# Kernel optimization log

Hardware: AMD Instinct MI355X
Metric: run time of the kernel (lower is better)

## Reference

```python
import jax, jax.numpy as jnp
import numpy as np

EMBED_DIM = 584  # module-global, used as softmax scale base (C ** -0.5)


def setup_inputs() -> dict:
    key = jax.random.key(0)
    ks = jax.random.split(key, 7)
    B, T, C, H, D = 16, 1024, 584, 8, 73
    x = jax.random.normal(ks[0], (B, T, C), dtype=jnp.float32)
    memory = jax.random.normal(ks[1], (B, T, C), dtype=jnp.float32)
    s = 0.02
    Wq = jax.random.normal(ks[2], (H, C, D), dtype=jnp.float32) * s
    Wk = jax.random.normal(ks[3], (H, C, D), dtype=jnp.float32) * s
    Wv = jax.random.normal(ks[4], (H, C, D), dtype=jnp.float32) * s
    Wp = jax.random.normal(ks[5], (C, C), dtype=jnp.float32) * s
    bp = jnp.zeros((C,), dtype=jnp.float32)
    return {"x": x, "memory": memory, "Wq": Wq, "Wk": Wk, "Wv": Wv, "Wp": Wp, "bp": bp}


def reference(x, memory, Wq, Wk, Wv, Wp, bp):
    B, T, C = x.shape
    # per-head projections, vectorized over heads: [B, H, T, D]
    q = jnp.einsum('btc,hcd->bhtd', x, Wq)
    k = jnp.einsum('bsc,hcd->bhsd', memory, Wk)
    v = jnp.einsum('btc,hcd->bhtd', x, Wv)  # NOTE: value from x, per original code
    # scale uses full embed dim C (not head size), per original code
    scores = jnp.einsum('bhtd,bhsd->bhts', q, k) * (C ** -0.5)
    weights = jax.nn.softmax(scores, axis=-1)
    # dropout is identity in eval/reference mode
    out = jnp.einsum('bhts,bhsd->bhtd', weights, v)  # requires S == T (matches original)
    out = out.transpose(0, 2, 1, 3).reshape(B, T, C)  # concat heads on last dim
    out = out @ Wp + bp  # output projection (dropout identity)
    return out
```

## Files before the change

kernel.cpp:

```cpp
#include <hip/hip_runtime.h>
#include <hip/hip_bf16.h>

typedef unsigned short u16;
typedef __attribute__((ext_vector_type(4))) unsigned short u16x4;
typedef __attribute__((ext_vector_type(8))) unsigned short u16x8;
typedef __attribute__((ext_vector_type(8))) __bf16 bf16x8;
typedef __attribute__((ext_vector_type(4))) float f32x4;

#define BB 16
#define TSEQ 1024
#define CC 584
#define HH 8
#define DHD 73
#define NR (BB*TSEQ)
#define KPW 640
#define DP 96
#define HD (HH*DP)
#define NP3 768
#define PPITCH 88
#define CEXP 0.0596985934f

__device__ __forceinline__ u16 f2bf(float f) {
  __bf16 h = (__bf16)f;
  return __builtin_bit_cast(u16, h);
}
__device__ __forceinline__ bf16x8 as_bf(u16x8 v) { return __builtin_bit_cast(bf16x8, v); }

#define GLL16(g, l) __builtin_amdgcn_global_load_lds( \
    (const __attribute__((address_space(1))) void*)(g), \
    (__attribute__((address_space(3))) void*)(l), 16, 0, 0)

#define BARRIER() asm volatile("s_barrier" ::: "memory")
#define VMW7()    asm volatile("s_waitcnt vmcnt(7)" ::: "memory")
#define VMW2()    asm volatile("s_waitcnt vmcnt(2)" ::: "memory")
#define VMW0()    asm volatile("s_waitcnt vmcnt(0)" ::: "memory")

#define PKA 10240
#define PKB2 720
#define PKC2 240
__global__ void pack_all_kernel(const float* __restrict__ x, const float* __restrict__ mem,
                                const float* __restrict__ Wq, const float* __restrict__ Wk,
                                const float* __restrict__ Wv, const float* __restrict__ Wp,
                                u16* __restrict__ xmb, u16* __restrict__ wt,
                                u16* __restrict__ wpt) {
  const int bidx = blockIdx.x;
  const int tid = threadIdx.x;
  if (bidx < PKA) {
    int idx = bidx * 256 + tid;
    int row = idx / (KPW / 8);
    int c8  = (idx % (KPW / 8)) * 8;
    u16x8 o = {0, 0, 0, 0, 0, 0, 0, 0};
    if (c8 < CC) {
      const float* src = (row < NR) ? &x[(size_t)row * CC + c8]
                                    : &mem[(size_t)(row - NR) * CC + c8];
      f32x4 a = *(const f32x4*)src;
      f32x4 b = *(const f32x4*)(src + 4);
#pragma unroll
      for (int t = 0; t < 4; t++) { o[t] = f2bf(a[t]); o[4 + t] = f2bf(b[t]); }
    }
    *(u16x8*)&xmb[(size_t)row * KPW + c8] = o;
  } else if (bidx < PKA + PKB2) {
    const int base = (bidx - PKA) * 2048 + tid;
#pragma unroll
    for (int e = 0; e < 8; e++) {
      int idx = base + e * 256;
      int w   = idx / (HD * KPW);
      int rem = idx % (HD * KPW);
      int n = rem / KPW;
      int k = rem % KPW;
      int h = n / DP, d = n % DP;
      u16 val = 0;
      if (d < DHD && k < CC) {
        const float* W = (w == 0) ? Wq : ((w == 1) ? Wv : Wk);
        val = f2bf(W[((size_t)h * CC + k) * DHD + d]);
      }
      wt[idx] = val;
    }
  } else {
    const int base = (bidx - PKA - PKB2) * 2048 + tid;
#pragma unroll
    for (int e = 0; e < 8; e++) {
      int idx = base + e * 256;
      int n = idx / KPW;
      int c = idx % KPW;
      u16 val = 0;
      if (n < CC && c < CC) val = f2bf(Wp[(size_t)c * CC + n]);
      wpt[idx] = val;
    }
  }
}


__device__ __forceinline__ void rd_a3(bf16x8 (&a)[4][2], const u16* lds, int base,
                                      int sw0, int sw1) {
#pragma unroll
  for (int mq = 0; mq < 4; mq++) {
    const int r = base + mq * 1024;
    a[mq][0] = as_bf(*(const u16x8*)&lds[r + sw0]);
    a[mq][1] = as_bf(*(const u16x8*)&lds[r + sw1]);
  }
}
__device__ __forceinline__ void rd_b3(bf16x8 (&b)[3][2], const u16* lds, int base,
                                      int sw0, int sw1) {
#pragma unroll
  for (int nq = 0; nq < 3; nq++) {
    const int r = base + nq * 1024;
    b[nq][0] = as_bf(*(const u16x8*)&lds[r + sw0]);
    b[nq][1] = as_bf(*(const u16x8*)&lds[r + sw1]);
  }
}
__device__ __forceinline__ void s_a1(const u16* gA, u16* ldst, int t, int lb) {
  GLL16(gA + (size_t)128 * KPW + (size_t)t * 64, ldst + lb + 8192);
  GLL16(gA + (size_t)192 * KPW + (size_t)t * 64, ldst + lb + 12288);
}
__device__ __forceinline__ void s_a0b(const u16* gA, const u16* gB, u16* ldst,
                                      int t, int lb) {
  GLL16(gA + (size_t)t * 64, ldst + lb);
  GLL16(gA + (size_t)64 * KPW + (size_t)t * 64, ldst + lb + 4096);
  GLL16(gB + (size_t)t * 64, ldst + lb + 16384);
  GLL16(gB + (size_t)64 * KPW + (size_t)t * 64, ldst + lb + 20480);
  GLL16(gB + (size_t)128 * KPW + (size_t)t * 64, ldst + lb + 24576);
}
__device__ __forceinline__ void mm43(f32x4 (&acc)[4][3], const bf16x8 (&a)[4][2],
                                     const bf16x8 (&b)[3][2]) {
  __builtin_amdgcn_s_setprio(1);
#pragma unroll
  for (int mq = 0; mq < 4; mq++)
#pragma unroll
    for (int nq = 0; nq < 3; nq++) {
      f32x4 c = acc[mq][nq];
      c = __builtin_amdgcn_mfma_f32_16x16x32_bf16(a[mq][0], b[nq][0], c, 0, 0, 0);
      c = __builtin_amdgcn_mfma_f32_16x16x32_bf16(a[mq][1], b[nq][1], c, 0, 0, 0);
      acc[mq][nq] = c;
    }
  __builtin_amdgcn_s_setprio(0);
}

template <int MODE>
__global__ __launch_bounds__(512, 2) void gemm8_kernel(
    const u16* __restrict__ A, const u16* __restrict__ Bt,
    void* __restrict__ CoutV, void* __restrict__ CoutV2,
    const float* __restrict__ bias) {
  extern __shared__ u16 lds[];
  const int tid  = threadIdx.x;
  const int lane = tid & 63;
  const int q15  = lane & 15;
  const int quad = lane >> 4;
  const int wave = tid >> 6;
  const int wmi  = wave >> 2;
  const int wni  = wave & 3;

  const int cpx = gridDim.x >> 3;
  const int bid = (blockIdx.x & 7) * cpx + (blockIdx.x >> 3);

  int m0, n0, npart;
  if (MODE == 4) {
    if (bid < 512) {
      m0 = (bid >> 3) * 256; int nt = bid & 7;
      n0 = nt * 192; npart = (nt >= 4) ? 1 : 0;
    } else {
      int b2 = bid - 512;
      m0 = NR + (b2 >> 2) * 256; n0 = 1536 + (b2 & 3) * 192; npart = 2;
    }
  } else {
    m0 = (bid >> 2) * 256; n0 = (bid & 3) * 192; npart = 0;
  }

  const int tr   = tid >> 3;
  const int scol = ((tid & 7) ^ (tr & 7)) * 8;
  const u16* gA = &A[(size_t)(m0 + tr) * KPW + scol];
  const u16* gB = &Bt[(size_t)(n0 + tr) * KPW + scol];
  u16* ldst = &lds[tid * 8];

  const int rb  = q15 & 7;
  const int sw0 = (quad ^ rb) * 8;
  const int sw1 = ((quad + 4) ^ rb) * 8;
  const int arow = (wmi * 64 + q15) * 64;
  const int brow = (wni * 48 + q15) * 64;

  f32x4 acc[2][4][3];
#pragma unroll
  for (int i = 0; i < 2; i++)
#pragma unroll
    for (int j = 0; j < 4; j++)
#pragma unroll
      for (int k = 0; k < 3; k++) acc[i][j][k] = (f32x4){0.f, 0.f, 0.f, 0.f};
  bf16x8 a[4][2], b[3][2];

  s_a0b(gA, gB, ldst, 0, 0);
  s_a1(gA, ldst, 0, 0);
  s_a0b(gA, gB, ldst, 1, 28672);
  VMW7(); BARRIER();

#pragma unroll 1
  for (int t = 0; t < 10; ++t) {
    const int lb = (t & 1) * 28672;
    const int lbo = lb ^ 28672;
    rd_a3(a, lds, lb + arow, sw0, sw1);
    rd_b3(b, lds, lb + 16384 + brow, sw0, sw1);
    if (t < 9) s_a1(gA, ldst, t + 1, lbo);
    if (t == 9) { VMW0(); } else { VMW7(); }
    BARRIER();
    mm43(acc[0], a, b);
    BARRIER();
    rd_a3(a, lds, lb + 8192 + arow, sw0, sw1);
    if (t < 8) { s_a0b(gA, gB, ldst, t + 2, lb); VMW7(); }
    else if (t == 8) { VMW2(); }
    BARRIER();
    mm43(acc[1], a, b);
    BARRIER();
  }

  const int rowb = m0 + wmi * 64 + quad * 4;
  const int colb = n0 + wni * 48 + q15;
#pragma unroll
  for (int mh = 0; mh < 2; mh++)
#pragma unroll
    for (int mq = 0; mq < 4; mq++)
#pragma unroll
      for (int nq = 0; nq < 3; nq++) {
        const f32x4 av = acc[mh][mq][nq];
        const int row = rowb + mh * 128 + mq * 16;
        const int col = colb + nq * 16;
        if (MODE == 4) {
          if (npart == 2) {
            u16* Cout = (u16*)CoutV2;
            const int rk = row - NR;
            const int ck = col - 1536;
#pragma unroll
            for (int r = 0; r < 4; r++)
              Cout[(size_t)(rk + r) * HD + ck] = f2bf(av[r]);
          } else if (npart == 0) {
            u16* Cout = (u16*)CoutV;
#pragma unroll
            for (int r = 0; r < 4; r++)
              Cout[(size_t)(row + r) * HD + col] = f2bf(av[r]);
          } else {
            u16* Cout = (u16*)CoutV;
            const int vn = col - HD;
            const int bb = row >> 10;
            const int tl = row & 1023;
            u16x4 pk;
#pragma unroll
            for (int r = 0; r < 4; r++) pk[r] = f2bf(av[r]);
            *(u16x4*)&Cout[(size_t)(NR * HD) + ((size_t)(bb * HD + vn)) * TSEQ + tl] = pk;
          }
        } else {
          if (col < CC) {
            float* Cout = (float*)CoutV;
            const float bvv = bias[col];
#pragma unroll
            for (int r = 0; r < 4; r++)
              Cout[(size_t)(row + r) * CC + col] = av[r] + bvv;
          }
        }
      }
}

__global__ __launch_bounds__(256, 3) void attn_kernel(
    const u16* __restrict__ qb, const u16* __restrict__ kb,
    const u16* __restrict__ vt, u16* __restrict__ attn) {
  __shared__ u16 smem[128 * 96 + 64 * 104 + 96 * 72];
  u16* Qs = smem;
  u16* Ks = smem + 128 * 96;
  u16* Vs = smem + 128 * 96 + 64 * 104;
  u16* Pt = smem;

  const int tid  = threadIdx.x;
  const int lane = tid & 63;
  const int wave = tid >> 6;
  const int q15  = lane & 15;
  const int quad = lane >> 4;
  const int bid  = blockIdx.x;
  const int loc  = bid >> 3;
  const int pair = (bid & 7) * 16 + (loc >> 3);
  const int b  = pair >> 3;
  const int h  = pair & 7;
  const int t0 = (loc & 7) * 128;
  const int wq0 = wave * 32;

  int krow[3], kc[3], vrow[3], vc[3];
#pragma unroll
  for (int p = 0; p < 3; p++) {
    int qk = tid + 256 * p;
    krow[p] = qk / 12; kc[p] = (qk % 12) * 8;
    int qv = tid + 256 * p;
    vrow[p] = qv / 8;  vc[p] = (qv % 8) * 8;
  }
  const u16* kbase = &kb[(size_t)(b * TSEQ) * HD + h * DP];
  const u16* vbase = &vt[(size_t)(b * HD + h * DP) * TSEQ];

  for (int q = tid; q < 128 * 12; q += 256) {
    int row = q / 12, c8 = (q % 12) * 8;
    *(u16x8*)&Qs[row * 96 + c8] =
        *(const u16x8*)&qb[(size_t)(b * TSEQ + t0 + row) * HD + h * DP + c8];
  }
  if (tid < 128) {
    const u16x8 z = {0, 0, 0, 0, 0, 0, 0, 0};
    size_t base = (size_t)(b * TSEQ + t0 + tid) * KPW + CC;
#pragma unroll
    for (int c = 0; c < (KPW - CC) / 8; c++) *(u16x8*)&attn[base + c * 8] = z;
  }
  __syncthreads();

  bf16x8 aq[2][3];
#pragma unroll
  for (int n = 0; n < 2; n++)
#pragma unroll
    for (int kcx = 0; kcx < 3; kcx++)
      aq[n][kcx] = as_bf(*(const u16x8*)&Qs[(wq0 + n * 16 + q15) * 96 + kcx * 32 + quad * 8]);

  float lsum[2] = {0.f, 0.f};
  f32x4 oacc[2][6];
#pragma unroll
  for (int m = 0; m < 2; m++)
#pragma unroll
    for (int jd = 0; jd < 6; jd++) oacc[m][jd] = (f32x4){0.f, 0.f, 0.f, 0.f};

  u16* Ptw = &Pt[wave * 32 * PPITCH];

  u16x8 kreg[3], vreg[3];
#pragma unroll
  for (int p = 0; p < 3; p++) {
    kreg[p] = *(const u16x8*)&kbase[(size_t)krow[p] * HD + kc[p]];
    vreg[p] = *(const u16x8*)&vbase[(size_t)vrow[p] * TSEQ + vc[p]];
  }

  for (int si = 0; si < 16; ++si) {
#pragma unroll
    for (int p = 0; p < 3; p++) {
      *(u16x8*)&Ks[krow[p] * 104 + kc[p]] = kreg[p];
      *(u16x8*)&Vs[vrow[p] * 72 + vc[p]]  = vreg[p];
    }
    __syncthreads();

    if (si < 15) {
      const int s1 = (si + 1) * 64;
#pragma unroll
      for (int p = 0; p < 3; p++) {
        kreg[p] = *(const u16x8*)&kbase[(size_t)(s1 + krow[p]) * HD + kc[p]];
        vreg[p] = *(const u16x8*)&vbase[(size_t)vrow[p] * TSEQ + s1 + vc[p]];
      }
    }

    f32x4 st[4][2];
#pragma unroll
    for (int mt = 0; mt < 4; mt++)
#pragma unroll
      for (int n = 0; n < 2; n++) st[mt][n] = (f32x4){0.f, 0.f, 0.f, 0.f};
#pragma unroll
    for (int kcx = 0; kcx < 3; kcx++) {
      bf16x8 ak[4];
#pragma unroll
      for (int mt = 0; mt < 4; mt++)
        ak[mt] = as_bf(*(const u16x8*)&Ks[(mt * 16 + q15) * 104 + kcx * 32 + quad * 8]);
#pragma unroll
      for (int mt = 0; mt < 4; mt++)
#pragma unroll
        for (int n = 0; n < 2; n++)
          st[mt][n] = __builtin_amdgcn_mfma_f32_16x16x32_bf16(ak[mt], aq[n][kcx], st[mt][n], 0, 0, 0);
    }

#pragma unroll
    for (int mt = 0; mt < 4; mt++)
#pragma unroll
      for (int n = 0; n < 2; n++) {
        f32x4 pv;
#pragma unroll
        for (int r = 0; r < 4; r++) pv[r] = __builtin_amdgcn_exp2f(st[mt][n][r] * CEXP);
        lsum[n] += (pv[0] + pv[1]) + (pv[2] + pv[3]);
        u16x4 pk;
#pragma unroll
        for (int r = 0; r < 4; r++) pk[r] = f2bf(pv[r]);
        *(u16x4*)&Ptw[(n * 16 + q15) * PPITCH + mt * 16 + quad * 4] = pk;
      }

#pragma unroll
    for (int kcx = 0; kcx < 2; kcx++) {
      bf16x8 ap[2];
#pragma unroll
      for (int m = 0; m < 2; m++)
        ap[m] = as_bf(*(const u16x8*)&Ptw[(m * 16 + q15) * PPITCH + kcx * 32 + quad * 8]);
#pragma unroll
      for (int jd = 0; jd < 6; jd++) {
        bf16x8 bv = as_bf(*(const u16x8*)&Vs[(jd * 16 + q15) * 72 + kcx * 32 + quad * 8]);
#pragma unroll
        for (int m = 0; m < 2; m++)
          oacc[m][jd] = __builtin_amdgcn_mfma_f32_16x16x32_bf16(ap[m], bv, oacc[m][jd], 0, 0, 0);
      }
    }
    __syncthreads();
  }

  float lr[2];
#pragma unroll
  for (int n = 0; n < 2; n++) {
    float s = lsum[n];
    s += __shfl_xor(s, 16);
    s += __shfl_xor(s, 32);
    lr[n] = s;
  }

#pragma unroll
  for (int m = 0; m < 2; m++) {
#pragma unroll
    for (int r = 0; r < 4; r++) {
      const float inv = 1.f / __shfl(lr[m], quad * 4 + r);
      const int trow = t0 + wq0 + m * 16 + quad * 4 + r;
#pragma unroll
      for (int jd = 0; jd < 5; jd++) {
        const int d = jd * 16 + q15;
        if (d < DHD)
          attn[(size_t)(b * TSEQ + trow) * KPW + h * DHD + d] = f2bf(oacc[m][jd][r] * inv);
      }
    }
  }
}


extern "C" void kernel_launch(void* const* d_in, const int* in_sizes, int n_in,
                              void* d_out, int out_size, void* d_ws, size_t ws_size,
                              hipStream_t stream) {
  const float* x   = (const float*)d_in[0];
  const float* mem = (const float*)d_in[1];
  const float* Wq  = (const float*)d_in[2];
  const float* Wk  = (const float*)d_in[3];
  const float* Wv  = (const float*)d_in[4];
  const float* Wp  = (const float*)d_in[5];
  const float* bp  = (const float*)d_in[6];
  float* out = (float*)d_out;

  char* ws = (char*)d_ws;
  const size_t SZ_XMB = (size_t)2 * NR * KPW * 2;
  const size_t SZ_WT  = (size_t)3 * HD * KPW * 2;
  const size_t SZ_WPT = (size_t)NP3 * KPW * 2;
  const size_t SZ_QB  = (size_t)NR * HD * 2;

  u16* xmb    = (u16*)(ws);
  u16* attn_o = (u16*)(ws);
  u16* wt     = (u16*)(ws + SZ_XMB);
  u16* wp_t   = (u16*)(ws + SZ_XMB + SZ_WT);
  u16* q_buf  = (u16*)(ws + SZ_XMB + SZ_WT + SZ_WPT);
  u16* vt_buf = q_buf + (size_t)NR * HD;
  u16* k_buf  = (u16*)(ws + SZ_XMB + SZ_WT + SZ_WPT + 2 * SZ_QB);

  (void)in_sizes; (void)n_in; (void)out_size; (void)ws_size;

  static bool s_attr = false;
  if (!s_attr) {
    (void)hipFuncSetAttribute((const void*)gemm8_kernel<4>,
                              hipFuncAttributeMaxDynamicSharedMemorySize, 114688);
    (void)hipFuncSetAttribute((const void*)gemm8_kernel<2>,
                              hipFuncAttributeMaxDynamicSharedMemorySize, 114688);
    s_attr = true;
  }

  pack_all_kernel<<<PKA + PKB2 + PKC2, 256, 0, stream>>>(x, mem, Wq, Wk, Wv, Wp,
                                                         xmb, wt, wp_t);

  gemm8_kernel<4><<<768, 512, 114688, stream>>>(xmb, wt, q_buf, k_buf, nullptr);

  attn_kernel<<<BB * HH * (TSEQ / 128), 256, 0, stream>>>(q_buf, k_buf, vt_buf, attn_o);

  gemm8_kernel<2><<<256, 512, 114688, stream>>>(attn_o, wp_t, out, nullptr, bp);
}
```

Before: 289.3 us.

## Shrink padded head dim from 96 to 80 across projection GEMM and attention

Head dimension padding drops from 96 to 80, so the QKV projection GEMM uses 128-wide N tiles (960 blocks, less LDS) and the attention kernel handles the 73-wide dot product as two full 32-K chunks plus a masked tail chunk. Q fragments are loaded straight from global memory into registers instead of staging through shared memory, and the shared-memory footprint shrinks. This cuts wasted padded FLOPs and bytes in the projection and attention, at the cost of smaller GEMM tiles with lower arithmetic intensity and some partially idle loads and MFMAs in the tail.

```diff
diff --git a/kernel.cpp b/kernel.cpp
--- a/kernel.cpp
+++ b/kernel.cpp
@@ -14,7 +14,7 @@
 #define DHD 73
 #define NR (BB*TSEQ)
 #define KPW 640
-#define DP 96
+#define DP 80
 #define HD (HH*DP)
 #define NP3 768
 #define PPITCH 88
@@ -32,11 +32,12 @@
 
 #define BARRIER() asm volatile("s_barrier" ::: "memory")
 #define VMW7()    asm volatile("s_waitcnt vmcnt(7)" ::: "memory")
+#define VMW6()    asm volatile("s_waitcnt vmcnt(6)" ::: "memory")
 #define VMW2()    asm volatile("s_waitcnt vmcnt(2)" ::: "memory")
 #define VMW0()    asm volatile("s_waitcnt vmcnt(0)" ::: "memory")
 
 #define PKA 10240
-#define PKB2 720
+#define PKB2 600
 #define PKC2 240
 __global__ void pack_all_kernel(const float* __restrict__ x, const float* __restrict__ mem,
                                 const float* __restrict__ Wq, const float* __restrict__ Wk,
@@ -91,7 +92,7 @@
 }
 
 
-__device__ __forceinline__ void rd_a3(bf16x8 (&a)[4][2], const u16* lds, int base,
+__device__ __forceinline__ void rd_a4(bf16x8 (&a)[4][2], const u16* lds, int base,
                                       int sw0, int sw1) {
 #pragma unroll
   for (int mq = 0; mq < 4; mq++) {
@@ -100,10 +101,11 @@
     a[mq][1] = as_bf(*(const u16x8*)&lds[r + sw1]);
   }
 }
-__device__ __forceinline__ void rd_b3(bf16x8 (&b)[3][2], const u16* lds, int base,
+template <int NQ>
+__device__ __forceinline__ void rd_bn(bf16x8 (&b)[NQ][2], const u16* lds, int base,
                                       int sw0, int sw1) {
 #pragma unroll
-  for (int nq = 0; nq < 3; nq++) {
+  for (int nq = 0; nq < NQ; nq++) {
     const int r = base + nq * 1024;
     b[nq][0] = as_bf(*(const u16x8*)&lds[r + sw0]);
     b[nq][1] = as_bf(*(const u16x8*)&lds[r + sw1]);
@@ -113,21 +115,23 @@
   GLL16(gA + (size_t)128 * KPW + (size_t)t * 64, ldst + lb + 8192);
   GLL16(gA + (size_t)192 * KPW + (size_t)t * 64, ldst + lb + 12288);
 }
+template <int NB>
 __device__ __forceinline__ void s_a0b(const u16* gA, const u16* gB, u16* ldst,
                                       int t, int lb) {
   GLL16(gA + (size_t)t * 64, ldst + lb);
   GLL16(gA + (size_t)64 * KPW + (size_t)t * 64, ldst + lb + 4096);
-  GLL16(gB + (size_t)t * 64, ldst + lb + 16384);
-  GLL16(gB + (size_t)64 * KPW + (size_t)t * 64, ldst + lb + 20480);
-  GLL16(gB + (size_t)128 * KPW + (size_t)t * 64, ldst + lb + 24576);
-}
-__device__ __forceinline__ void mm43(f32x4 (&acc)[4][3], const bf16x8 (&a)[4][2],
-                                     const bf16x8 (&b)[3][2]) {
+#pragma unroll
+  for (int u = 0; u < NB; u++)
+    GLL16(gB + (size_t)(u * 64) * KPW + (size_t)t * 64, ldst + lb + 16384 + u * 4096);
+}
+template <int NQ>
+__device__ __forceinline__ void mm4n(f32x4 (&acc)[4][NQ], const bf16x8 (&a)[4][2],
+                                     const bf16x8 (&b)[NQ][2]) {
   __builtin_amdgcn_s_setprio(1);
 #pragma unroll
   for (int mq = 0; mq < 4; mq++)
 #pragma unroll
-    for (int nq = 0; nq < 3; nq++) {
+    for (int nq = 0; nq < NQ; nq++) {
       f32x4 c = acc[mq][nq];
       c = __builtin_amdgcn_mfma_f32_16x16x32_bf16(a[mq][0], b[nq][0], c, 0, 0, 0);
       c = __builtin_amdgcn_mfma_f32_16x16x32_bf16(a[mq][1], b[nq][1], c, 0, 0, 0);
@@ -141,6 +145,10 @@
     const u16* __restrict__ A, const u16* __restrict__ Bt,
     void* __restrict__ CoutV, void* __restrict__ CoutV2,
     const float* __restrict__ bias) {
+  constexpr int NB = (MODE == 4) ? 2 : 3;
+  constexpr int NQ = NB;
+  constexpr int WN = NQ * 16;
+  constexpr int SB = 16384 + NB * 4096;
   extern __shared__ u16 lds[];
   const int tid  = threadIdx.x;
   const int lane = tid & 63;
@@ -155,12 +163,13 @@
 
   int m0, n0, npart;
   if (MODE == 4) {
-    if (bid < 512) {
-      m0 = (bid >> 3) * 256; int nt = bid & 7;
-      n0 = nt * 192; npart = (nt >= 4) ? 1 : 0;
+    if (bid < 640) {
+      m0 = (bid / 10) * 256; int nt = bid % 10;
+      if (nt < 5) { n0 = nt * 128; npart = 0; }
+      else        { n0 = 640 + (nt - 5) * 128; npart = 1; }
     } else {
-      int b2 = bid - 512;
-      m0 = NR + (b2 >> 2) * 256; n0 = 1536 + (b2 & 3) * 192; npart = 2;
+      int b2 = bid - 640;
+      m0 = NR + (b2 / 5) * 256; n0 = 1280 + (b2 % 5) * 128; npart = 2;
     }
   } else {
     m0 = (bid >> 2) * 256; n0 = (bid & 3) * 192; npart = 0;
@@ -176,49 +185,51 @@
   const int sw0 = (quad ^ rb) * 8;
   const int sw1 = ((quad + 4) ^ rb) * 8;
   const int arow = (wmi * 64 + q15) * 64;
-  const int brow = (wni * 48 + q15) * 64;
-
-  f32x4 acc[2][4][3];
+  const int brow = (wni * WN + q15) * 64;
+
+  f32x4 acc[2][4][NQ];
 #pragma unroll
   for (int i = 0; i < 2; i++)
 #pragma unroll
     for (int j = 0; j < 4; j++)
 #pragma unroll
-      for (int k = 0; k < 3; k++) acc[i][j][k] = (f32x4){0.f, 0.f, 0.f, 0.f};
-  bf16x8 a[4][2], b[3][2];
-
-  s_a0b(gA, gB, ldst, 0, 0);
+      for (int k = 0; k < NQ; k++) acc[i][j][k] = (f32x4){0.f, 0.f, 0.f, 0.f};
+  bf16x8 a[4][2], b[NQ][2];
+
+  s_a0b<NB>(gA, gB, ldst, 0, 0);
   s_a1(gA, ldst, 0, 0);
-  s_a0b(gA, gB, ldst, 1, 28672);
-  VMW7(); BARRIER();
+  s_a0b<NB>(gA, gB, ldst, 1, SB);
+  if constexpr (NB == 2) VMW6(); else VMW7();
+  BARRIER();
 
 #pragma unroll 1
   for (int t = 0; t < 10; ++t) {
-    const int lb = (t & 1) * 28672;
-    const int lbo = lb ^ 28672;
-    rd_a3(a, lds, lb + arow, sw0, sw1);
-    rd_b3(b, lds, lb + 16384 + brow, sw0, sw1);
+    const int lb = (t & 1) * SB;
+    const int lbo = lb ^ SB;
+    rd_a4(a, lds, lb + arow, sw0, sw1);
+    rd_bn<NQ>(b, lds, lb + 16384 + brow, sw0, sw1);
     if (t < 9) s_a1(gA, ldst, t + 1, lbo);
-    if (t == 9) { VMW0(); } else { VMW7(); }
+    if (t == 9) { VMW0(); } else { if constexpr (NB == 2) VMW6(); else VMW7(); }
     BARRIER();
-    mm43(acc[0], a, b);
+    mm4n<NQ>(acc[0], a, b);
     BARRIER();
-    rd_a3(a, lds, lb + 8192 + arow, sw0, sw1);
-    if (t < 8) { s_a0b(gA, gB, ldst, t + 2, lb); VMW7(); }
+    rd_a4(a, lds, lb + 8192 + arow, sw0, sw1);
+    if (t < 8) { s_a0b<NB>(gA, gB, ldst, t + 2, lb);
+                 if constexpr (NB == 2) VMW6(); else VMW7(); }
     else if (t == 8) { VMW2(); }
     BARRIER();
-    mm43(acc[1], a, b);
+    mm4n<NQ>(acc[1], a, b);
     BARRIER();
   }
 
   const int rowb = m0 + wmi * 64 + quad * 4;
-  const int colb = n0 + wni * 48 + q15;
+  const int colb = n0 + wni * WN + q15;
 #pragma unroll
   for (int mh = 0; mh < 2; mh++)
 #pragma unroll
     for (int mq = 0; mq < 4; mq++)
 #pragma unroll
-      for (int nq = 0; nq < 3; nq++) {
+      for (int nq = 0; nq < NQ; nq++) {
         const f32x4 av = acc[mh][mq][nq];
         const int row = rowb + mh * 128 + mq * 16;
         const int col = colb + nq * 16;
@@ -226,7 +237,7 @@
           if (npart == 2) {
             u16* Cout = (u16*)CoutV2;
             const int rk = row - NR;
-            const int ck = col - 1536;
+            const int ck = col - 1280;
 #pragma unroll
             for (int r = 0; r < 4; r++)
               Cout[(size_t)(rk + r) * HD + ck] = f2bf(av[r]);
@@ -237,7 +248,7 @@
               Cout[(size_t)(row + r) * HD + col] = f2bf(av[r]);
           } else {
             u16* Cout = (u16*)CoutV;
-            const int vn = col - HD;
+            const int vn = col - 640;
             const int bb = row >> 10;
             const int tl = row & 1023;
             u16x4 pk;
@@ -260,11 +271,10 @@
 __global__ __launch_bounds__(256, 3) void attn_kernel(
     const u16* __restrict__ qb, const u16* __restrict__ kb,
     const u16* __restrict__ vt, u16* __restrict__ attn) {
-  __shared__ u16 smem[128 * 96 + 64 * 104 + 96 * 72];
-  u16* Qs = smem;
-  u16* Ks = smem + 128 * 96;
-  u16* Vs = smem + 128 * 96 + 64 * 104;
+  __shared__ u16 smem[11264 + 64 * 88 + 80 * 72];
   u16* Pt = smem;
+  u16* Ks = smem + 11264;
+  u16* Vs = smem + 11264 + 64 * 88;
 
   const int tid  = threadIdx.x;
   const int lane = tid & 63;
@@ -278,69 +288,83 @@
   const int h  = pair & 7;
   const int t0 = (loc & 7) * 128;
   const int wq0 = wave * 32;
+  const bool w3 = (tid < 128);
 
   int krow[3], kc[3], vrow[3], vc[3];
 #pragma unroll
   for (int p = 0; p < 3; p++) {
     int qk = tid + 256 * p;
-    krow[p] = qk / 12; kc[p] = (qk % 12) * 8;
-    int qv = tid + 256 * p;
-    vrow[p] = qv / 8;  vc[p] = (qv % 8) * 8;
+    krow[p] = qk / 10; kc[p] = (qk % 10) * 8;
+    vrow[p] = qk >> 3; vc[p] = (qk & 7) * 8;
   }
   const u16* kbase = &kb[(size_t)(b * TSEQ) * HD + h * DP];
   const u16* vbase = &vt[(size_t)(b * HD + h * DP) * TSEQ];
 
-  for (int q = tid; q < 128 * 12; q += 256) {
-    int row = q / 12, c8 = (q % 12) * 8;
-    *(u16x8*)&Qs[row * 96 + c8] =
-        *(const u16x8*)&qb[(size_t)(b * TSEQ + t0 + row) * HD + h * DP + c8];
-  }
+  bf16x8 aq[2][2], aqt[2];
+  {
+    const u16x8 z = {0, 0, 0, 0, 0, 0, 0, 0};
+#pragma unroll
+    for (int n = 0; n < 2; n++) {
+      const size_t qrow = (size_t)(b * TSEQ + t0 + wq0 + n * 16 + q15) * HD + h * DP;
+#pragma unroll
+      for (int kcx = 0; kcx < 2; kcx++)
+        aq[n][kcx] = as_bf(*(const u16x8*)&qb[qrow + kcx * 32 + quad * 8]);
+      u16x8 tload = z;
+      if (quad < 2) tload = *(const u16x8*)&qb[qrow + 64 + quad * 8];
+      aqt[n] = as_bf(tload);
+    }
+  }
+
   if (tid < 128) {
     const u16x8 z = {0, 0, 0, 0, 0, 0, 0, 0};
     size_t base = (size_t)(b * TSEQ + t0 + tid) * KPW + CC;
 #pragma unroll
     for (int c = 0; c < (KPW - CC) / 8; c++) *(u16x8*)&attn[base + c * 8] = z;
   }
-  __syncthreads();
-
-  bf16x8 aq[2][3];
-#pragma unroll
-  for (int n = 0; n < 2; n++)
-#pragma unroll
-    for (int kcx = 0; kcx < 3; kcx++)
-      aq[n][kcx] = as_bf(*(const u16x8*)&Qs[(wq0 + n * 16 + q15) * 96 + kcx * 32 + quad * 8]);
 
   float lsum[2] = {0.f, 0.f};
-  f32x4 oacc[2][6];
+  f32x4 oacc[2][5];
 #pragma unroll
   for (int m = 0; m < 2; m++)
 #pragma unroll
-    for (int jd = 0; jd < 6; jd++) oacc[m][jd] = (f32x4){0.f, 0.f, 0.f, 0.f};
+    for (int jd = 0; jd < 5; jd++) oacc[m][jd] = (f32x4){0.f, 0.f, 0.f, 0.f};
 
   u16* Ptw = &Pt[wave * 32 * PPITCH];
 
   u16x8 kreg[3], vreg[3];
 #pragma unroll
-  for (int p = 0; p < 3; p++) {
+  for (int p = 0; p < 2; p++) {
     kreg[p] = *(const u16x8*)&kbase[(size_t)krow[p] * HD + kc[p]];
     vreg[p] = *(const u16x8*)&vbase[(size_t)vrow[p] * TSEQ + vc[p]];
   }
+  if (w3) {
+    kreg[2] = *(const u16x8*)&kbase[(size_t)krow[2] * HD + kc[2]];
+    vreg[2] = *(const u16x8*)&vbase[(size_t)vrow[2] * TSEQ + vc[2]];
+  }
 
   for (int si = 0; si < 16; ++si) {
 #pragma unroll
-    for (int p = 0; p < 3; p++) {
-      *(u16x8*)&Ks[krow[p] * 104 + kc[p]] = kreg[p];
-      *(u16x8*)&Vs[vrow[p] * 72 + vc[p]]  = vreg[p];
+    for (int p = 0; p < 2; p++) {
+      *(u16x8*)&Ks[krow[p] * 88 + kc[p]] = kreg[p];
+      *(u16x8*)&Vs[vrow[p] * 72 + vc[p]] = vreg[p];
+    }
+    if (w3) {
+      *(u16x8*)&Ks[krow[2] * 88 + kc[2]] = kreg[2];
+      *(u16x8*)&Vs[vrow[2] * 72 + vc[2]] = vreg[2];
     }
     __syncthreads();
 
     if (si < 15) {
       const int s1 = (si + 1) * 64;
 #pragma unroll
-      for (int p = 0; p < 3; p++) {
+      for (int p = 0; p < 2; p++) {
         kreg[p] = *(const u16x8*)&kbase[(size_t)(s1 + krow[p]) * HD + kc[p]];
         vreg[p] = *(const u16x8*)&vbase[(size_t)vrow[p] * TSEQ + s1 + vc[p]];
       }
+      if (w3) {
+        kreg[2] = *(const u16x8*)&kbase[(size_t)(s1 + krow[2]) * HD + kc[2]];
+        vreg[2] = *(const u16x8*)&vbase[(size_t)vrow[2] * TSEQ + s1 + vc[2]];
+      }
     }
 
     f32x4 st[4][2];
@@ -349,16 +373,28 @@
 #pragma unroll
       for (int n = 0; n < 2; n++) st[mt][n] = (f32x4){0.f, 0.f, 0.f, 0.f};
 #pragma unroll
-    for (int kcx = 0; kcx < 3; kcx++) {
+    for (int kcx = 0; kcx < 2; kcx++) {
       bf16x8 ak[4];
 #pragma unroll
       for (int mt = 0; mt < 4; mt++)
-        ak[mt] = as_bf(*(const u16x8*)&Ks[(mt * 16 + q15) * 104 + kcx * 32 + quad * 8]);
+        ak[mt] = as_bf(*(const u16x8*)&Ks[(mt * 16 + q15) * 88 + kcx * 32 + quad * 8]);
 #pragma unroll
       for (int mt = 0; mt < 4; mt++)
 #pragma unroll
         for (int n = 0; n < 2; n++)
           st[mt][n] = __builtin_amdgcn_mfma_f32_16x16x32_bf16(ak[mt], aq[n][kcx], st[mt][n], 0, 0, 0);
+    }
+    {
+      const u16x8 z = {0, 0, 0, 0, 0, 0, 0, 0};
+#pragma unroll
+      for (int mt = 0; mt < 4; mt++) {
+        u16x8 tl = z;
+        if (quad < 2) tl = *(const u16x8*)&Ks[(mt * 16 + q15) * 88 + 64 + quad * 8];
+        bf16x8 akt = as_bf(tl);
+#pragma unroll
+        for (int n = 0; n < 2; n++)
+          st[mt][n] = __builtin_amdgcn_mfma_f32_16x16x32_bf16(akt, aqt[n], st[mt][n], 0, 0, 0);
+      }
     }
 
 #pragma unroll
@@ -382,7 +418,7 @@
       for (int m = 0; m < 2; m++)
         ap[m] = as_bf(*(const u16x8*)&Ptw[(m * 16 + q15) * PPITCH + kcx * 32 + quad * 8]);
 #pragma unroll
-      for (int jd = 0; jd < 6; jd++) {
+      for (int jd = 0; jd < 5; jd++) {
         bf16x8 bv = as_bf(*(const u16x8*)&Vs[(jd * 16 + q15) * 72 + kcx * 32 + quad * 8]);
 #pragma unroll
         for (int m = 0; m < 2; m++)
@@ -458,7 +494,7 @@
   pack_all_kernel<<<PKA + PKB2 + PKC2, 256, 0, stream>>>(x, mem, Wq, Wk, Wv, Wp,
                                                          xmb, wt, wp_t);
 
-  gemm8_kernel<4><<<768, 512, 114688, stream>>>(xmb, wt, q_buf, k_buf, nullptr);
+  gemm8_kernel<4><<<960, 512, 98304, stream>>>(xmb, wt, q_buf, k_buf, nullptr);
 
   attn_kernel<<<BB * HH * (TSEQ / 128), 256, 0, stream>>>(q_buf, k_buf, vt_buf, attn_o);
 
```

After: 286.9 us. Within noise of the previous version (-0.8%).
